# Optimization experiments

Measured on AMD Instinct MI355X. Metric: run time of the kernel, lower is better.

## Reference

```python
import jax, jax.numpy as jnp
import numpy as np

N = 8192
D = 128
AVG_DEG = 32


def setup_inputs() -> dict:
    key = jax.random.key(0)
    ks = jax.random.split(key, 10)
    Z = jax.random.normal(ks[0], (N, D), dtype=jnp.float32)
    # random symmetric binary adjacency with avg degree ~ AVG_DEG
    p = AVG_DEG / N
    adj = (jax.random.uniform(ks[1], (N, N)) < p).astype(jnp.float32)
    adj = jnp.maximum(adj, adj.T)
    # symmetric normalized adjacency: D^{-1/2} A D^{-1/2}
    deg = adj.sum(axis=1)
    d_inv_sqrt = jnp.where(deg > 0, 1.0 / jnp.sqrt(deg), 0.0)
    A_norm = d_inv_sqrt[:, None] * adj * d_inv_sqrt[None, :]
    sc = 1.0 / np.sqrt(D)
    W_D = jax.random.uniform(ks[2], (D, D), minval=-sc, maxval=sc, dtype=jnp.float32)
    W_C = jax.random.uniform(ks[3], (D, D), minval=-sc, maxval=sc, dtype=jnp.float32)
    w_V = jax.random.uniform(ks[4], (D,), minval=-sc, maxval=sc, dtype=jnp.float32)
    W1 = jax.random.uniform(ks[5], (D, D), minval=-sc, maxval=sc, dtype=jnp.float32)
    b1 = jax.random.uniform(ks[6], (D,), minval=-sc, maxval=sc, dtype=jnp.float32)
    W2 = jax.random.uniform(ks[7], (D, D), minval=-sc, maxval=sc, dtype=jnp.float32)
    b2 = jax.random.uniform(ks[8], (D,), minval=-sc, maxval=sc, dtype=jnp.float32)
    omega_logit = jnp.float32(0.0)  # sigmoid -> 0.5
    delta_logit = jnp.float32(0.0)
    return {"Z": Z, "A_norm": A_norm, "W_D": W_D, "W_C": W_C, "w_V": w_V,
            "W1": W1, "b1": b1, "W2": W2, "b2": b2,
            "omega_logit": omega_logit, "delta_logit": delta_logit}


def reference(Z, A_norm, W_D, W_C, w_V, W1, b1, W2, b2, omega_logit, delta_logit):
    omega = jax.nn.sigmoid(omega_logit)
    delta = jax.nn.sigmoid(delta_logit)
    # Diffusion: ReLU(A_norm @ Z @ W_D^T)
    dif = jax.nn.relu(A_norm @ (Z @ W_D.T))  # [N, D]
    # Convection (standard attention). Since W_V is D->1,
    # W_V(z_i - z_j) == s_i - s_j with s = Z @ w_V -> avoid [N,N,D] tensor.
    s = Z @ w_V                                   # [N]
    V_bar = jax.nn.sigmoid(s[:, None] - s[None, :])  # [N, N]
    A = jax.nn.softmax(V_bar, axis=1)                # row-stochastic [N, N]
    con = A @ (Z @ W_C.T)                            # [N, D]
    # Reaction: nonlinear MLP
    rea = jnp.tanh(Z @ W1.T + b1) @ W2.T + b2        # [N, D]
    return omega * dif + (1.0 - omega) * con + delta * rea
```

## Files before the change

### kernel.cpp

```cpp
#include <hip/hip_runtime.h>
#include <hip/hip_bf16.h>
#include <stdint.h>

#define NN 8192
#define DD 128
#define CAP 160

typedef float f32x4 __attribute__((ext_vector_type(4)));
typedef unsigned int u32x4 __attribute__((ext_vector_type(4)));
typedef unsigned short u16x4 __attribute__((ext_vector_type(4)));
typedef __bf16 bf16x8 __attribute__((ext_vector_type(8)));
typedef __bf16 bf16x4 __attribute__((ext_vector_type(4)));

__device__ __forceinline__ f32x4 mfma16(bf16x8 a, bf16x8 b, f32x4 c) {
    return __builtin_amdgcn_mfma_f32_16x16x32_bf16(a, b, c, 0, 0, 0);
}

__device__ __forceinline__ bf16x8 pack8(f32x4 lo, f32x4 hi) {
    bf16x8 r;
    r[0] = (__bf16)lo[0]; r[1] = (__bf16)lo[1]; r[2] = (__bf16)lo[2]; r[3] = (__bf16)lo[3];
    r[4] = (__bf16)hi[0]; r[5] = (__bf16)hi[1]; r[6] = (__bf16)hi[2]; r[7] = (__bf16)hi[3];
    return r;
}

__device__ __forceinline__ float fast_sigmoid(float x) {
    return __builtin_amdgcn_rcpf(1.0f + __expf(-x));
}

__global__ __launch_bounds__(256) void k_scan2(
    const float* __restrict__ A, const float* __restrict__ Z,
    const float* __restrict__ wV, const float* __restrict__ W_D,
    const float* __restrict__ W_C, const float* __restrict__ W1,
    const float* __restrict__ W2, uint32_t* __restrict__ mask,
    float* __restrict__ dsq, float* __restrict__ E, __bf16* __restrict__ Wb)
{
    const int w = threadIdx.x >> 6, l = threadIdx.x & 63;
    const int row = blockIdx.x * 4 + w;

    const float* rp = A + (size_t)row * NN + l * 4;
    uint32_t* mrow = mask + (size_t)row * 256;
    uint32_t dcnt = 0;
    #pragma unroll
    for (int g = 0; g < 4; ++g) {
        uint32_t mw = 0;
        #pragma unroll
        for (int t = 0; t < 8; ++t) {
            const f32x4 v = *(const f32x4*)(rp + (g * 8 + t) * 256);
            const uint32_t nb = (v[0] != 0.f ? 1u : 0u) | (v[1] != 0.f ? 2u : 0u)
                              | (v[2] != 0.f ? 4u : 0u) | (v[3] != 0.f ? 8u : 0u);
            mw |= nb << (t * 4);
        }
        mrow[g * 64 + l] = mw;
        dcnt += __popc(mw);
    }
    #pragma unroll
    for (int off = 32; off > 0; off >>= 1) dcnt += __shfl_xor((int)dcnt, off, 64);
    if (l == 0) dsq[row] = (dcnt > 0) ? 1.0f / sqrtf((float)dcnt) : 0.0f;

    float p = Z[row * DD + l] * wV[l] + Z[row * DD + 64 + l] * wV[64 + l];
    #pragma unroll
    for (int off = 32; off > 0; off >>= 1) p += __shfl_xor(p, off, 64);
    if (l == 0) E[row] = __expf(p);

    const int t = blockIdx.x * 256 + threadIdx.x;
    if (t < 16384) {
        const int m = t >> 12, i = t & 4095;
        const float* src = (m == 0) ? W_D : (m == 1) ? W_C : (m == 2) ? W1 : W2;
        const f32x4 v = *(const f32x4*)(src + i * 4);
        bf16x4 b;
        b[0] = (__bf16)v[0]; b[1] = (__bf16)v[1]; b[2] = (__bf16)v[2]; b[3] = (__bf16)v[3];
        *(bf16x4*)(Wb + m * 16384 + i * 4) = b;
    }
}

__global__ __launch_bounds__(256) void k_prep2(
    const float* __restrict__ Z, const __bf16* __restrict__ Wb,
    const float* __restrict__ b1, const float* __restrict__ b2,
    const float* __restrict__ delta_logit, const float* __restrict__ dsq,
    __bf16* __restrict__ XR, __bf16* __restrict__ YB, __bf16* __restrict__ REA)
{
    __shared__ __bf16 Hs[32][136];
    const int tid = threadIdx.x;
    const int w = tid >> 6, l = tid & 63;
    const int lr = l & 15, lg = l >> 4;
    const int wr = w & 1, wn = w >> 1;
    const int r0 = blockIdx.x * 32;
    const int arow = r0 + 16 * wr + lr;
    const __bf16* WDb = Wb;
    const __bf16* WCb = Wb + 16384;
    const __bf16* W1b = Wb + 32768;
    const __bf16* W2b = Wb + 49152;

    const f32x4 zero4 = {0.f, 0.f, 0.f, 0.f};
    f32x4 aXD[4], aY[4], aH[4];
    #pragma unroll
    for (int i = 0; i < 4; ++i) { aXD[i] = zero4; aY[i] = zero4; aH[i] = zero4; }

    #pragma unroll
    for (int t = 0; t < 4; ++t) {
        const int k0 = 32 * t + 8 * lg;
        const bf16x8 af = pack8(*(const f32x4*)(Z + arow * DD + k0),
                                *(const f32x4*)(Z + arow * DD + k0 + 4));
        #pragma unroll
        for (int nf = 0; nf < 4; ++nf) {
            const int col = 64 * wn + 16 * nf + lr;
            aXD[nf] = mfma16(af, *(const bf16x8*)(WDb + col * DD + k0), aXD[nf]);
            aY[nf]  = mfma16(af, *(const bf16x8*)(WCb + col * DD + k0), aY[nf]);
            aH[nf]  = mfma16(af, *(const bf16x8*)(W1b + col * DD + k0), aH[nf]);
        }
    }

    const int orow = r0 + 16 * wr + 4 * lg;
    const int tile = orow >> 5;
    const f32x4 dsq4 = *(const f32x4*)(dsq + orow);
    #pragma unroll
    for (int nf = 0; nf < 4; ++nf) {
        const int col = 64 * wn + 16 * nf + lr;
        bf16x4 yo;
        const float bb1 = b1[col];
        #pragma unroll
        for (int r = 0; r < 4; ++r) {
            XR[(orow + r) * DD + col] = (__bf16)(aXD[nf][r] * dsq4[r]);
            yo[r] = (__bf16)aY[nf][r];
            const float x = aH[nf][r] + bb1;
            const float e = __expf(2.0f * x);
            Hs[16 * wr + 4 * lg + r][col] = (__bf16)(1.0f - 2.0f * __builtin_amdgcn_rcpf(e + 1.0f));
        }
        *(bf16x4*)(YB + tile * 4096 + col * 32 + (orow & 31)) = yo;
    }
    __syncthreads();

    f32x4 aR[4];
    #pragma unroll
    for (int i = 0; i < 4; ++i) aR[i] = zero4;
    #pragma unroll
    for (int t = 0; t < 4; ++t) {
        const int k0 = 32 * t + 8 * lg;
        const bf16x8 hf = *(const bf16x8*)(&Hs[16 * wr + lr][k0]);
        #pragma unroll
        for (int nf = 0; nf < 4; ++nf) {
            const int col = 64 * wn + 16 * nf + lr;
            aR[nf] = mfma16(hf, *(const bf16x8*)(W2b + col * DD + k0), aR[nf]);
        }
    }
    const float delta = fast_sigmoid(delta_logit[0]);
    #pragma unroll
    for (int nf = 0; nf < 4; ++nf) {
        const int col = 64 * wn + 16 * nf + lr;
        const float bb2 = b2[col];
        #pragma unroll
        for (int r = 0; r < 4; ++r)
            REA[(orow + r) * DD + col] = (__bf16)(delta * (aR[nf][r] + bb2));
    }
}

__global__ __launch_bounds__(512) __attribute__((amdgpu_waves_per_eu(2, 2))) void k_main(
    const uint32_t* __restrict__ mask, const float* __restrict__ E,
    const __bf16* __restrict__ YB, const __bf16* __restrict__ XR,
    const __bf16* __restrict__ REA, const float* __restrict__ dsq,
    const float* __restrict__ omega_logit, float* __restrict__ out)
{
    __shared__ float red[4][64][76];
    __shared__ uint16_t ents16[32][CAP];
    __shared__ uint32_t cnt32[32];
    float* conS = &red[0][0][0];
    const int tid = threadIdx.x;
    const int w = tid >> 6, l = tid & 63;
    const int lr = l & 15, lg = l >> 4;
    const int r0 = blockIdx.x * 32;
    const int row = tid >> 4;
    const int g16 = tid & 15;

    if (tid < 32) cnt32[tid] = 0;
    __syncthreads();
    {
        const uint32_t* mrow = mask + (size_t)(r0 + row) * 256 + g16 * 16;
        #pragma unroll
        for (int q = 0; q < 4; ++q) {
            const u32x4 mv = *(const u32x4*)(mrow + q * 4);
            #pragma unroll
            for (int s = 0; s < 4; ++s) {
                uint32_t m = mv[s];
                const int widx = g16 * 16 + q * 4 + s;
                const int cbase = (widx >> 6) * 8;
                const int coff = (widx & 63) * 4;
                while (m) {
                    const int b = __ffs(m) - 1; m &= m - 1;
                    const int col = (cbase + (b >> 2)) * 256 + coff + (b & 3);
                    const uint32_t slot = atomicAdd(&cnt32[row], 1u);
                    if (slot < CAP) ents16[row][slot] = (uint16_t)col;
                }
            }
        }
    }

    const int kstart = w * 1024;
    const float* ep = E + kstart + 8 * lg;
    const __bf16* yp = YB + (kstart >> 5) * 4096 + lr * 32 + 8 * lg;
    const float u0 = E[r0 + lr];
    const float u1 = E[r0 + 16 + lr];

    const f32x4 zero4 = {0.f, 0.f, 0.f, 0.f};
    f32x4 aC0[8], aC1[8], aden0 = zero4, aden1 = zero4;
    #pragma unroll
    for (int i = 0; i < 8; ++i) { aC0[i] = zero4; aC1[i] = zero4; }
    bf16x8 ones;
    #pragma unroll
    for (int i = 0; i < 8; ++i) ones[i] = (__bf16)1.0f;

    f32x4 eAa, eBa, eAb, eBb;
    bf16x8 bya[8], byb[8];
    intptr_t adv = 32;

#define LOADT(S) do {                                                         \
        eA##S = *(const f32x4*)(ep); eB##S = *(const f32x4*)(ep + 4);         \
        _Pragma("unroll")                                                     \
        for (int c = 0; c < 8; ++c) by##S[c] = *(const bf16x8*)(yp + c * 512);\
        ep += adv; yp += adv * 128;                                           \
    } while (0)

#define COMPT(S) do {                                                         \
        bf16x8 gf0, gf1;                                                      \
        _Pragma("unroll")                                                     \
        for (int j = 0; j < 4; ++j) {                                         \
            const float ea = eA##S[j], eb = eB##S[j];                         \
            gf0[j]     = (__bf16)__expf(u0 * __builtin_amdgcn_rcpf(u0 + ea)); \
            gf0[4 + j] = (__bf16)__expf(u0 * __builtin_amdgcn_rcpf(u0 + eb)); \
            gf1[j]     = (__bf16)__expf(u1 * __builtin_amdgcn_rcpf(u1 + ea)); \
            gf1[4 + j] = (__bf16)__expf(u1 * __builtin_amdgcn_rcpf(u1 + eb)); \
        }                                                                     \
        _Pragma("unroll")                                                     \
        for (int c = 0; c < 8; ++c) {                                         \
            aC0[c] = mfma16(gf0, by##S[c], aC0[c]);                           \
            aC1[c] = mfma16(gf1, by##S[c], aC1[c]);                           \
        }                                                                     \
        aden0 = mfma16(gf0, ones, aden0);                                     \
        aden1 = mfma16(gf1, ones, aden1);                                     \
    } while (0)

    LOADT(a);
    for (int it = 0; it < 16; ++it) {
        if (it == 15) adv = 0;
        LOADT(b); COMPT(a);
        LOADT(a); COMPT(b);
    }
#undef LOADT
#undef COMPT

#define STORE_ACC(dst) do {                                                   \
        _Pragma("unroll")                                                     \
        for (int c = 0; c < 8; ++c) {                                         \
            *(f32x4*)((dst) + c * 4)      = aC0[c];                           \
            *(f32x4*)((dst) + 36 + c * 4) = aC1[c];                           \
        }                                                                     \
        *(f32x4*)((dst) + 32)      = aden0;                                   \
        *(f32x4*)((dst) + 36 + 32) = aden1;                                   \
    } while (0)
#define ADD_ACC(src) do {                                                     \
        _Pragma("unroll")                                                     \
        for (int c = 0; c < 8; ++c) {                                         \
            aC0[c] += *(const f32x4*)((src) + c * 4);                         \
            aC1[c] += *(const f32x4*)((src) + 36 + c * 4);                    \
        }                                                                     \
        aden0 += *(const f32x4*)((src) + 32);                                 \
        aden1 += *(const f32x4*)((src) + 36 + 32);                            \
    } while (0)

    __syncthreads();
    if (w >= 4) STORE_ACC(&red[w - 4][l][0]);
    __syncthreads();
    if (w < 4) ADD_ACC(&red[w][l][0]);
    __syncthreads();
    if (w == 2 || w == 3) STORE_ACC(&red[w - 2][l][0]);
    __syncthreads();
    if (w < 2) ADD_ACC(&red[w][l][0]);
    __syncthreads();
    if (w == 1) STORE_ACC(&red[0][l][0]);
    __syncthreads();
    if (w == 0) {
        ADD_ACC(&red[0][l][0]);
        __builtin_amdgcn_s_barrier();
        #pragma unroll
        for (int rf = 0; rf < 2; ++rf) {
            #pragma unroll
            for (int c = 0; c < 8; ++c) {
                const f32x4 v = rf ? aC1[c] : aC0[c];
                #pragma unroll
                for (int r = 0; r < 4; ++r)
                    conS[(16 * rf + 4 * lg + r) * 132 + 16 * c + lr] = v[r];
            }
            if (lr == 0) {
                const f32x4 d = rf ? aden1 : aden0;
                #pragma unroll
                for (int r = 0; r < 4; ++r)
                    conS[32 * 132 + 16 * rf + 4 * lg + r] = d[r];
            }
        }
    } else {
        __builtin_amdgcn_s_barrier();
    }
    __syncthreads();

    const int col0 = 8 * g16;
    const int rg = r0 + row;
    float acc[8];
    #pragma unroll
    for (int i = 0; i < 8; ++i) acc[i] = 0.0f;

    const uint32_t n = min(cnt32[row], (uint32_t)CAP);
    uint32_t e = 0;
    for (; e + 4 <= n; e += 4) {
        const u16x4 p = *(const u16x4*)(&ents16[row][e]);
        const bf16x8 x0 = *(const bf16x8*)(XR + (size_t)p[0] * DD + col0);
        const bf16x8 x1 = *(const bf16x8*)(XR + (size_t)p[1] * DD + col0);
        const bf16x8 x2 = *(const bf16x8*)(XR + (size_t)p[2] * DD + col0);
        const bf16x8 x3 = *(const bf16x8*)(XR + (size_t)p[3] * DD + col0);
        #pragma unroll
        for (int i = 0; i < 8; ++i)
            acc[i] += (float)x0[i] + (float)x1[i] + (float)x2[i] + (float)x3[i];
    }
    for (; e < n; ++e) {
        const bf16x8 xv = *(const bf16x8*)(XR + (size_t)ents16[row][e] * DD + col0);
        #pragma unroll
        for (int i = 0; i < 8; ++i) acc[i] += (float)xv[i];
    }

    const float omega = fast_sigmoid(omega_logit[0]);
    const float om1 = 1.0f - omega;
    const float dsqi = dsq[rg];
    const float dinv = __builtin_amdgcn_rcpf(conS[32 * 132 + row]);
    const bf16x8 rea8 = *(const bf16x8*)(REA + (size_t)rg * DD + col0);
    f32x4 o0, o1;
    #pragma unroll
    for (int i = 0; i < 8; ++i) {
        const float dv = fmaxf(dsqi * acc[i], 0.0f);
        const float cv = conS[row * 132 + col0 + i] * dinv;
        const float v = (float)rea8[i] + omega * dv + om1 * cv;
        if (i < 4) o0[i] = v; else o1[i - 4] = v;
    }
    *(f32x4*)(out + (size_t)rg * DD + col0) = o0;
    *(f32x4*)(out + (size_t)rg * DD + col0 + 4) = o1;
}

extern "C" void kernel_launch(void* const* d_in, const int* in_sizes, int n_in,
                              void* d_out, int out_size, void* d_ws, size_t ws_size,
                              hipStream_t stream) {
    (void)in_sizes; (void)n_in; (void)out_size; (void)ws_size;
    const float* Z   = (const float*)d_in[0];
    const float* A   = (const float*)d_in[1];
    const float* W_D = (const float*)d_in[2];
    const float* W_C = (const float*)d_in[3];
    const float* wV  = (const float*)d_in[4];
    const float* W1  = (const float*)d_in[5];
    const float* b1  = (const float*)d_in[6];
    const float* W2  = (const float*)d_in[7];
    const float* b2  = (const float*)d_in[8];
    const float* omega_logit = (const float*)d_in[9];
    const float* delta_logit = (const float*)d_in[10];
    float* out = (float*)d_out;

    char* wsb = (char*)d_ws;
    float*    E    = (float*)wsb;
    __bf16*   Wb   = (__bf16*)(wsb + 32768);
    __bf16*   XR   = (__bf16*)(wsb + 163840);
    __bf16*   YB   = (__bf16*)(wsb + 163840 + 2097152);
    __bf16*   REA  = (__bf16*)(wsb + 163840 + 2 * 2097152);
    float*    dsq  = (float*)(wsb + 163840 + 3 * 2097152);
    uint32_t* mask = (uint32_t*)(wsb + 163840 + 3 * 2097152 + 32768);

    k_scan2<<<dim3(2048), dim3(256), 0, stream>>>(A, Z, wV, W_D, W_C, W1, W2,
                                                  mask, dsq, E, Wb);
    k_prep2<<<dim3(256), dim3(256), 0, stream>>>(Z, Wb, b1, b2, delta_logit, dsq,
                                                 XR, YB, REA);
    k_main<<<dim3(256), dim3(512), 0, stream>>>(mask, E, YB, XR, REA, dsq,
                                                omega_logit, out);
}
```

Baseline: 437.1 us.

## Overlap adjacency scan with convection attention in one interleaved kernel

Adds a merged kernel whose blocks are split by block index: four of every five scan the dense adjacency into a bitmask and degrees, while the fifth computes the convection softmax-weighted product over 16 rows with MFMA. The intent is to run the memory-bound scan of the 256 MB adjacency at the same time as the compute-bound attention instead of serially. Because dsq is no longer known when XR is produced, the degree scaling moves into the gather loop of the final kernel as per-neighbour dsq loads, and the separate denominator MFMA is replaced with a scalar sum. Convection results now round-trip through global memory in fp32, and there is an extra small weight-conversion launch.

```diff
diff --git a/kernel.cpp b/kernel.cpp
--- a/kernel.cpp
+++ b/kernel.cpp
@@ -27,57 +27,26 @@
     return __builtin_amdgcn_rcpf(1.0f + __expf(-x));
 }
 
-__global__ __launch_bounds__(256) void k_scan2(
-    const float* __restrict__ A, const float* __restrict__ Z,
-    const float* __restrict__ wV, const float* __restrict__ W_D,
-    const float* __restrict__ W_C, const float* __restrict__ W1,
-    const float* __restrict__ W2, uint32_t* __restrict__ mask,
-    float* __restrict__ dsq, float* __restrict__ E, __bf16* __restrict__ Wb)
+__global__ __launch_bounds__(256) void k_conv_w(
+    const float* __restrict__ W_D, const float* __restrict__ W_C,
+    const float* __restrict__ W1, const float* __restrict__ W2,
+    __bf16* __restrict__ Wb)
 {
-    const int w = threadIdx.x >> 6, l = threadIdx.x & 63;
-    const int row = blockIdx.x * 4 + w;
-
-    const float* rp = A + (size_t)row * NN + l * 4;
-    uint32_t* mrow = mask + (size_t)row * 256;
-    uint32_t dcnt = 0;
-    #pragma unroll
-    for (int g = 0; g < 4; ++g) {
-        uint32_t mw = 0;
-        #pragma unroll
-        for (int t = 0; t < 8; ++t) {
-            const f32x4 v = *(const f32x4*)(rp + (g * 8 + t) * 256);
-            const uint32_t nb = (v[0] != 0.f ? 1u : 0u) | (v[1] != 0.f ? 2u : 0u)
-                              | (v[2] != 0.f ? 4u : 0u) | (v[3] != 0.f ? 8u : 0u);
-            mw |= nb << (t * 4);
-        }
-        mrow[g * 64 + l] = mw;
-        dcnt += __popc(mw);
-    }
-    #pragma unroll
-    for (int off = 32; off > 0; off >>= 1) dcnt += __shfl_xor((int)dcnt, off, 64);
-    if (l == 0) dsq[row] = (dcnt > 0) ? 1.0f / sqrtf((float)dcnt) : 0.0f;
-
-    float p = Z[row * DD + l] * wV[l] + Z[row * DD + 64 + l] * wV[64 + l];
-    #pragma unroll
-    for (int off = 32; off > 0; off >>= 1) p += __shfl_xor(p, off, 64);
-    if (l == 0) E[row] = __expf(p);
-
     const int t = blockIdx.x * 256 + threadIdx.x;
-    if (t < 16384) {
-        const int m = t >> 12, i = t & 4095;
-        const float* src = (m == 0) ? W_D : (m == 1) ? W_C : (m == 2) ? W1 : W2;
-        const f32x4 v = *(const f32x4*)(src + i * 4);
-        bf16x4 b;
-        b[0] = (__bf16)v[0]; b[1] = (__bf16)v[1]; b[2] = (__bf16)v[2]; b[3] = (__bf16)v[3];
-        *(bf16x4*)(Wb + m * 16384 + i * 4) = b;
-    }
+    const int m = t >> 12, i = t & 4095;
+    const float* src = (m == 0) ? W_D : (m == 1) ? W_C : (m == 2) ? W1 : W2;
+    const f32x4 v = *(const f32x4*)(src + i * 4);
+    bf16x4 b;
+    b[0] = (__bf16)v[0]; b[1] = (__bf16)v[1]; b[2] = (__bf16)v[2]; b[3] = (__bf16)v[3];
+    *(bf16x4*)(Wb + m * 16384 + i * 4) = b;
 }
 
 __global__ __launch_bounds__(256) void k_prep2(
-    const float* __restrict__ Z, const __bf16* __restrict__ Wb,
-    const float* __restrict__ b1, const float* __restrict__ b2,
-    const float* __restrict__ delta_logit, const float* __restrict__ dsq,
-    __bf16* __restrict__ XR, __bf16* __restrict__ YB, __bf16* __restrict__ REA)
+    const float* __restrict__ Z, const float* __restrict__ wV,
+    const __bf16* __restrict__ Wb, const float* __restrict__ b1,
+    const float* __restrict__ b2, const float* __restrict__ delta_logit,
+    float* __restrict__ E, __bf16* __restrict__ XR, __bf16* __restrict__ YB,
+    __bf16* __restrict__ REA)
 {
     __shared__ __bf16 Hs[32][136];
     const int tid = threadIdx.x;
@@ -85,6 +54,24 @@
     const int lr = l & 15, lg = l >> 4;
     const int wr = w & 1, wn = w >> 1;
     const int r0 = blockIdx.x * 32;
+
+    {
+        const int erow = r0 + (tid >> 3);
+        const int e0 = (tid & 7) * 16;
+        const float* zp = Z + erow * DD + e0;
+        float p = 0.f;
+        #pragma unroll
+        for (int q = 0; q < 4; ++q) {
+            const f32x4 zv = *(const f32x4*)(zp + 4 * q);
+            const f32x4 wv = *(const f32x4*)(wV + e0 + 4 * q);
+            p += zv[0] * wv[0] + zv[1] * wv[1] + zv[2] * wv[2] + zv[3] * wv[3];
+        }
+        p += __shfl_xor(p, 4, 64);
+        p += __shfl_xor(p, 2, 64);
+        p += __shfl_xor(p, 1, 64);
+        if ((tid & 7) == 0) E[erow] = __expf(p);
+    }
+
     const int arow = r0 + 16 * wr + lr;
     const __bf16* WDb = Wb;
     const __bf16* WCb = Wb + 16384;
@@ -112,7 +99,6 @@
 
     const int orow = r0 + 16 * wr + 4 * lg;
     const int tile = orow >> 5;
-    const f32x4 dsq4 = *(const f32x4*)(dsq + orow);
     #pragma unroll
     for (int nf = 0; nf < 4; ++nf) {
         const int col = 64 * wn + 16 * nf + lr;
@@ -120,7 +106,7 @@
         const float bb1 = b1[col];
         #pragma unroll
         for (int r = 0; r < 4; ++r) {
-            XR[(orow + r) * DD + col] = (__bf16)(aXD[nf][r] * dsq4[r]);
+            XR[(orow + r) * DD + col] = (__bf16)aXD[nf][r];
             yo[r] = (__bf16)aY[nf][r];
             const float x = aH[nf][r] + bb1;
             const float e = __expf(2.0f * x);
@@ -154,24 +140,142 @@
     }
 }
 
-__global__ __launch_bounds__(512) __attribute__((amdgpu_waves_per_eu(2, 2))) void k_main(
-    const uint32_t* __restrict__ mask, const float* __restrict__ E,
-    const __bf16* __restrict__ YB, const __bf16* __restrict__ XR,
+__global__ __launch_bounds__(256) __attribute__((amdgpu_waves_per_eu(4)))
+void k_merge(const float* __restrict__ A, const float* __restrict__ E,
+             const __bf16* __restrict__ YB, uint32_t* __restrict__ mask,
+             float* __restrict__ dsq, float* __restrict__ CON,
+             float* __restrict__ den)
+{
+    __shared__ float red[2][64][40];
+    const int bid = blockIdx.x;
+    const int tid = threadIdx.x;
+    const int w = tid >> 6, l = tid & 63;
+
+    if (bid % 5 != 0) {
+        const int sidx = bid - bid / 5 - 1;
+        const int row = sidx * 4 + w;
+        const float* rp = A + (size_t)row * NN + l * 4;
+        uint32_t* mrow = mask + (size_t)row * 256;
+        uint32_t dcnt = 0;
+        #pragma unroll
+        for (int g = 0; g < 4; ++g) {
+            uint32_t mw = 0;
+            #pragma unroll
+            for (int t = 0; t < 8; ++t) {
+                const f32x4 v = *(const f32x4*)(rp + (g * 8 + t) * 256);
+                const uint32_t nb = (v[0] != 0.f ? 1u : 0u) | (v[1] != 0.f ? 2u : 0u)
+                                  | (v[2] != 0.f ? 4u : 0u) | (v[3] != 0.f ? 8u : 0u);
+                mw |= nb << (t * 4);
+            }
+            mrow[g * 64 + l] = mw;
+            dcnt += __popc(mw);
+        }
+        #pragma unroll
+        for (int off = 32; off > 0; off >>= 1) dcnt += __shfl_xor((int)dcnt, off, 64);
+        if (l == 0) dsq[row] = (dcnt > 0) ? 1.0f / sqrtf((float)dcnt) : 0.0f;
+        return;
+    }
+
+    const int cid = bid / 5;
+    const int r0 = cid * 16;
+    const int lr = l & 15, lg = l >> 4;
+    const int kstart = w * 2048;
+    const float* ep = E + kstart + 8 * lg;
+    const __bf16* yp = YB + (kstart >> 5) * 4096 + lr * 32 + 8 * lg;
+    const float u0 = E[r0 + lr];
+
+    const f32x4 zero4 = {0.f, 0.f, 0.f, 0.f};
+    f32x4 aC[8];
+    #pragma unroll
+    for (int i = 0; i < 8; ++i) aC[i] = zero4;
+    float dn = 0.f;
+
+    f32x4 eAa, eBa, eAb, eBb;
+    bf16x8 bya[8], byb[8];
+    intptr_t adv = 32;
+
+#define LOADT(S) do {                                                         \
+        eA##S = *(const f32x4*)(ep); eB##S = *(const f32x4*)(ep + 4);         \
+        _Pragma("unroll")                                                     \
+        for (int c = 0; c < 8; ++c) by##S[c] = *(const bf16x8*)(yp + c * 512);\
+        ep += adv; yp += adv * 128;                                           \
+    } while (0)
+
+#define COMPT(S) do {                                                         \
+        bf16x8 gf;                                                            \
+        _Pragma("unroll")                                                     \
+        for (int j = 0; j < 4; ++j) {                                         \
+            const float s0 = u0 * __builtin_amdgcn_rcpf(u0 + eA##S[j]);       \
+            const float s1 = u0 * __builtin_amdgcn_rcpf(u0 + eB##S[j]);       \
+            const float g0 = __expf(s0), g1 = __expf(s1);                     \
+            gf[j] = (__bf16)g0; gf[4 + j] = (__bf16)g1;                       \
+            dn += g0 + g1;                                                    \
+        }                                                                     \
+        _Pragma("unroll")                                                     \
+        for (int c = 0; c < 8; ++c) aC[c] = mfma16(gf, by##S[c], aC[c]);      \
+    } while (0)
+
+    LOADT(a);
+    for (int it = 0; it < 32; ++it) {
+        if (it == 31) adv = 0;
+        LOADT(b); COMPT(a);
+        LOADT(a); COMPT(b);
+    }
+#undef LOADT
+#undef COMPT
+
+    __syncthreads();
+    if (w >= 2) {
+        float* s = &red[w - 2][l][0];
+        #pragma unroll
+        for (int c = 0; c < 8; ++c) *(f32x4*)(s + 4 * c) = aC[c];
+        s[32] = dn;
+    }
+    __syncthreads();
+    if (w < 2) {
+        const float* s = &red[w][l][0];
+        #pragma unroll
+        for (int c = 0; c < 8; ++c) aC[c] += *(const f32x4*)(s + 4 * c);
+        dn += s[32];
+    }
+    __syncthreads();
+    if (w == 1) {
+        float* s = &red[0][l][0];
+        #pragma unroll
+        for (int c = 0; c < 8; ++c) *(f32x4*)(s + 4 * c) = aC[c];
+        s[32] = dn;
+    }
+    __syncthreads();
+    if (w == 0) {
+        const float* s = &red[0][l][0];
+        #pragma unroll
+        for (int c = 0; c < 8; ++c) aC[c] += *(const f32x4*)(s + 4 * c);
+        dn += s[32];
+        dn += __shfl_xor(dn, 16, 64);
+        dn += __shfl_xor(dn, 32, 64);
+        #pragma unroll
+        for (int c = 0; c < 8; ++c) {
+            #pragma unroll
+            for (int r = 0; r < 4; ++r)
+                CON[(size_t)(r0 + 4 * lg + r) * DD + 16 * c + lr] = aC[c][r];
+        }
+        if (l < 16) den[r0 + l] = dn;
+    }
+}
+
+__global__ __launch_bounds__(256) void k_fin(
+    const uint32_t* __restrict__ mask, const __bf16* __restrict__ XR,
     const __bf16* __restrict__ REA, const float* __restrict__ dsq,
+    const float* __restrict__ CON, const float* __restrict__ den,
     const float* __restrict__ omega_logit, float* __restrict__ out)
 {
-    __shared__ float red[4][64][76];
-    __shared__ uint16_t ents16[32][CAP];
-    __shared__ uint32_t cnt32[32];
-    float* conS = &red[0][0][0];
+    __shared__ uint16_t ents16[16][CAP];
+    __shared__ uint32_t cnt32[16];
     const int tid = threadIdx.x;
-    const int w = tid >> 6, l = tid & 63;
-    const int lr = l & 15, lg = l >> 4;
-    const int r0 = blockIdx.x * 32;
-    const int row = tid >> 4;
-    const int g16 = tid & 15;
-
-    if (tid < 32) cnt32[tid] = 0;
+    const int r0 = blockIdx.x * 16;
+    const int row = tid >> 4, g16 = tid & 15;
+
+    if (tid < 16) cnt32[tid] = 0;
     __syncthreads();
     {
         const uint32_t* mrow = mask + (size_t)(r0 + row) * 256 + g16 * 16;
@@ -193,112 +297,6 @@
             }
         }
     }
-
-    const int kstart = w * 1024;
-    const float* ep = E + kstart + 8 * lg;
-    const __bf16* yp = YB + (kstart >> 5) * 4096 + lr * 32 + 8 * lg;
-    const float u0 = E[r0 + lr];
-    const float u1 = E[r0 + 16 + lr];
-
-    const f32x4 zero4 = {0.f, 0.f, 0.f, 0.f};
-    f32x4 aC0[8], aC1[8], aden0 = zero4, aden1 = zero4;
-    #pragma unroll
-    for (int i = 0; i < 8; ++i) { aC0[i] = zero4; aC1[i] = zero4; }
-    bf16x8 ones;
-    #pragma unroll
-    for (int i = 0; i < 8; ++i) ones[i] = (__bf16)1.0f;
-
-    f32x4 eAa, eBa, eAb, eBb;
-    bf16x8 bya[8], byb[8];
-    intptr_t adv = 32;
-
-#define LOADT(S) do {                                                         \
-        eA##S = *(const f32x4*)(ep); eB##S = *(const f32x4*)(ep + 4);         \
-        _Pragma("unroll")                                                     \
-        for (int c = 0; c < 8; ++c) by##S[c] = *(const bf16x8*)(yp + c * 512);\
-        ep += adv; yp += adv * 128;                                           \
-    } while (0)
-
-#define COMPT(S) do {                                                         \
-        bf16x8 gf0, gf1;                                                      \
-        _Pragma("unroll")                                                     \
-        for (int j = 0; j < 4; ++j) {                                         \
-            const float ea = eA##S[j], eb = eB##S[j];                         \
-            gf0[j]     = (__bf16)__expf(u0 * __builtin_amdgcn_rcpf(u0 + ea)); \
-            gf0[4 + j] = (__bf16)__expf(u0 * __builtin_amdgcn_rcpf(u0 + eb)); \
-            gf1[j]     = (__bf16)__expf(u1 * __builtin_amdgcn_rcpf(u1 + ea)); \
-            gf1[4 + j] = (__bf16)__expf(u1 * __builtin_amdgcn_rcpf(u1 + eb)); \
-        }                                                                     \
-        _Pragma("unroll")                                                     \
-        for (int c = 0; c < 8; ++c) {                                         \
-            aC0[c] = mfma16(gf0, by##S[c], aC0[c]);                           \
-            aC1[c] = mfma16(gf1, by##S[c], aC1[c]);                           \
-        }                                                                     \
-        aden0 = mfma16(gf0, ones, aden0);                                     \
-        aden1 = mfma16(gf1, ones, aden1);                                     \
-    } while (0)
-
-    LOADT(a);
-    for (int it = 0; it < 16; ++it) {
-        if (it == 15) adv = 0;
-        LOADT(b); COMPT(a);
-        LOADT(a); COMPT(b);
-    }
-#undef LOADT
-#undef COMPT
-
-#define STORE_ACC(dst) do {                                                   \
-        _Pragma("unroll")                                                     \
-        for (int c = 0; c < 8; ++c) {                                         \
-            *(f32x4*)((dst) + c * 4)      = aC0[c];                           \
-            *(f32x4*)((dst) + 36 + c * 4) = aC1[c];                           \
-        }                                                                     \
-        *(f32x4*)((dst) + 32)      = aden0;                                   \
-        *(f32x4*)((dst) + 36 + 32) = aden1;                                   \
-    } while (0)
-#define ADD_ACC(src) do {                                                     \
-        _Pragma("unroll")                                                     \
-        for (int c = 0; c < 8; ++c) {                                         \
-            aC0[c] += *(const f32x4*)((src) + c * 4);                         \
-            aC1[c] += *(const f32x4*)((src) + 36 + c * 4);                    \
-        }                                                                     \
-        aden0 += *(const f32x4*)((src) + 32);                                 \
-        aden1 += *(const f32x4*)((src) + 36 + 32);                            \
-    } while (0)
-
-    __syncthreads();
-    if (w >= 4) STORE_ACC(&red[w - 4][l][0]);
-    __syncthreads();
-    if (w < 4) ADD_ACC(&red[w][l][0]);
-    __syncthreads();
-    if (w == 2 || w == 3) STORE_ACC(&red[w - 2][l][0]);
-    __syncthreads();
-    if (w < 2) ADD_ACC(&red[w][l][0]);
-    __syncthreads();
-    if (w == 1) STORE_ACC(&red[0][l][0]);
-    __syncthreads();
-    if (w == 0) {
-        ADD_ACC(&red[0][l][0]);
-        __builtin_amdgcn_s_barrier();
-        #pragma unroll
-        for (int rf = 0; rf < 2; ++rf) {
-            #pragma unroll
-            for (int c = 0; c < 8; ++c) {
-                const f32x4 v = rf ? aC1[c] : aC0[c];
-                #pragma unroll
-                for (int r = 0; r < 4; ++r)
-                    conS[(16 * rf + 4 * lg + r) * 132 + 16 * c + lr] = v[r];
-            }
-            if (lr == 0) {
-                const f32x4 d = rf ? aden1 : aden0;
-                #pragma unroll
-                for (int r = 0; r < 4; ++r)
-                    conS[32 * 132 + 16 * rf + 4 * lg + r] = d[r];
-            }
-        }
-    } else {
-        __builtin_amdgcn_s_barrier();
-    }
     __syncthreads();
 
     const int col0 = 8 * g16;
@@ -311,30 +309,35 @@
     uint32_t e = 0;
     for (; e + 4 <= n; e += 4) {
         const u16x4 p = *(const u16x4*)(&ents16[row][e]);
+        const float d0 = dsq[p[0]], d1 = dsq[p[1]], d2 = dsq[p[2]], d3 = dsq[p[3]];
         const bf16x8 x0 = *(const bf16x8*)(XR + (size_t)p[0] * DD + col0);
         const bf16x8 x1 = *(const bf16x8*)(XR + (size_t)p[1] * DD + col0);
         const bf16x8 x2 = *(const bf16x8*)(XR + (size_t)p[2] * DD + col0);
         const bf16x8 x3 = *(const bf16x8*)(XR + (size_t)p[3] * DD + col0);
         #pragma unroll
         for (int i = 0; i < 8; ++i)
-            acc[i] += (float)x0[i] + (float)x1[i] + (float)x2[i] + (float)x3[i];
+            acc[i] += d0 * (float)x0[i] + d1 * (float)x1[i]
+                    + d2 * (float)x2[i] + d3 * (float)x3[i];
     }
     for (; e < n; ++e) {
-        const bf16x8 xv = *(const bf16x8*)(XR + (size_t)ents16[row][e] * DD + col0);
-        #pragma unroll
-        for (int i = 0; i < 8; ++i) acc[i] += (float)xv[i];
+        const uint16_t pc = ents16[row][e];
+        const float dv = dsq[pc];
+        const bf16x8 xv = *(const bf16x8*)(XR + (size_t)pc * DD + col0);
+        #pragma unroll
+        for (int i = 0; i < 8; ++i) acc[i] += dv * (float)xv[i];
     }
 
     const float omega = fast_sigmoid(omega_logit[0]);
     const float om1 = 1.0f - omega;
     const float dsqi = dsq[rg];
-    const float dinv = __builtin_amdgcn_rcpf(conS[32 * 132 + row]);
+    const float dinv = __builtin_amdgcn_rcpf(den[rg]);
     const bf16x8 rea8 = *(const bf16x8*)(REA + (size_t)rg * DD + col0);
+    const float* cp = CON + (size_t)rg * DD + col0;
     f32x4 o0, o1;
     #pragma unroll
     for (int i = 0; i < 8; ++i) {
         const float dv = fmaxf(dsqi * acc[i], 0.0f);
-        const float cv = conS[row * 132 + col0 + i] * dinv;
+        const float cv = cp[i] * dinv;
         const float v = (float)rea8[i] + omega * dv + om1 * cv;
         if (i < 4) o0[i] = v; else o1[i - 4] = v;
     }
@@ -363,15 +366,17 @@
     float*    E    = (float*)wsb;
     __bf16*   Wb   = (__bf16*)(wsb + 32768);
     __bf16*   XR   = (__bf16*)(wsb + 163840);
-    __bf16*   YB   = (__bf16*)(wsb + 163840 + 2097152);
-    __bf16*   REA  = (__bf16*)(wsb + 163840 + 2 * 2097152);
-    float*    dsq  = (float*)(wsb + 163840 + 3 * 2097152);
-    uint32_t* mask = (uint32_t*)(wsb + 163840 + 3 * 2097152 + 32768);
-
-    k_scan2<<<dim3(2048), dim3(256), 0, stream>>>(A, Z, wV, W_D, W_C, W1, W2,
-                                                  mask, dsq, E, Wb);
-    k_prep2<<<dim3(256), dim3(256), 0, stream>>>(Z, Wb, b1, b2, delta_logit, dsq,
-                                                 XR, YB, REA);
-    k_main<<<dim3(256), dim3(512), 0, stream>>>(mask, E, YB, XR, REA, dsq,
-                                                omega_logit, out);
-}
+    __bf16*   YB   = (__bf16*)(wsb + 2260992);
+    __bf16*   REA  = (__bf16*)(wsb + 4358144);
+    float*    dsq  = (float*)(wsb + 6455296);
+    uint32_t* mask = (uint32_t*)(wsb + 6488064);
+    float*    CON  = (float*)(wsb + 14876672);
+    float*    den  = (float*)(wsb + 19070976);
+
+    k_conv_w<<<dim3(64), dim3(256), 0, stream>>>(W_D, W_C, W1, W2, Wb);
+    k_prep2<<<dim3(256), dim3(256), 0, stream>>>(Z, wV, Wb, b1, b2, delta_logit,
+                                                 E, XR, YB, REA);
+    k_merge<<<dim3(2560), dim3(256), 0, stream>>>(A, E, YB, mask, dsq, CON, den);
+    k_fin<<<dim3(512), dim3(256), 0, stream>>>(mask, XR, REA, dsq, CON, den,
+                                               omega_logit, out);
+}
```

After: 507.7 us. +16.2%, slower.
